# Kernel tuning notes

Measured on AMD Instinct MI355X. Metric: run time of the kernel, lower is better.

The kernel has to match this reference:

```python
import jax, jax.numpy as jnp
import numpy as np

B, K, U, I, D = 16384, 64, 100000, 100000, 256

def setup_inputs() -> dict:
    key = jax.random.key(0)
    k1, k2, k3, k4, k5, k6, k7, k8 = jax.random.split(key, 8)
    return {
        "nodes_u": jax.random.randint(k1, (B,), 0, U),
        "nodes_v": jax.random.randint(k2, (B,), 0, I),
        "neighbors": jax.random.randint(k3, (B, K), 0, U),
        "neighbor_counts": jax.random.randint(k4, (B,), 0, K + 1),
        "u2e": jax.random.normal(k5, (U, D), dtype=jnp.float32),
        "v2e": jax.random.normal(k6, (I, D), dtype=jnp.float32),
        "W": jax.random.normal(k7, (D, 2 * D), dtype=jnp.float32) * 0.05,  # torch Linear weight [out, in]
        "b": jax.random.normal(k8, (D,), dtype=jnp.float32) * 0.05,
    }

def reference(nodes_u, nodes_v, neighbors, neighbor_counts, u2e, v2e, W, b):
    # self embeddings [B, D]
    self_emb = u2e[nodes_u]
    # gather padded neighbor embeddings [B, K, D]
    neib_emb = u2e[neighbors]
    k_ = neighbors.shape[1]
    mask = jnp.arange(k_)[None, :] < neighbor_counts[:, None]          # [B, K] valid-neighbor mask
    nsum = jnp.einsum('bkd,bk->bd', neib_emb, mask.astype(neib_emb.dtype))
    cnt = jnp.maximum(neighbor_counts, 1).astype(self_emb.dtype)[:, None]
    nmean = nsum / cnt                                                  # mean-pool over valid neighbors
    cat = jnp.concatenate([self_emb, nmean], axis=1)                    # [B, 2D]
    proj = cat @ W.T + b                                                # Linear(2D -> D)
    # users with no neighbors use raw self embedding (matches `if len(neibs) > 0` branch)
    uemb = jnp.where((neighbor_counts > 0)[:, None], proj, self_emb)
    scores = jnp.sum(uemb * v2e[nodes_v], axis=1)                       # [B]
    return scores
```

## Files before the change

### kernel.cpp

```cpp
#include <hip/hip_runtime.h>

#define B_ROWS   16384
#define K_NB     64
#define D_DIM    256
#define TWO_D    512
#define R_BLK    8
#define THREADS  256

__global__ __launch_bounds__(THREADS, 4)
void easyrec_fused(const int* __restrict__ nodes_u,
                   const int* __restrict__ nodes_v,
                   const int* __restrict__ neighbors,
                   const int* __restrict__ neighbor_counts,
                   const float* __restrict__ u2e,
                   const float* __restrict__ v2e,
                   const float* __restrict__ W,
                   const float* __restrict__ bias,
                   float* __restrict__ out)
{
    __shared__ __align__(16) int   nbr_lds[R_BLK * K_NB];
    __shared__ __align__(16) float cat_lds[R_BLK][TWO_D];
    __shared__ float red_lds[R_BLK * 4];
    __shared__ float selfdot_lds[R_BLK];
    __shared__ float bdot_lds[R_BLK];

    const int t    = threadIdx.x;
    const int wave = t >> 6;
    const int lane = t & 63;
    const int row0 = blockIdx.x * R_BLK;

    nbr_lds[t]           = neighbors[(size_t)row0 * K_NB + t];
    nbr_lds[t + THREADS] = neighbors[(size_t)row0 * K_NB + t + THREADS];
    __syncthreads();

    const unsigned colb = (unsigned)lane * 16u;

    {
        const float4 b4 = *(const float4*)((const char*)bias + colb);
        #pragma unroll
        for (int rr = 0; rr < 2; ++rr) {
            const int r   = wave + rr * 4;
            const int row = row0 + r;
            const int nu  = __builtin_amdgcn_readfirstlane(nodes_u[row]);
            const int nv  = __builtin_amdgcn_readfirstlane(nodes_v[row]);
            const float4 self4 = *(const float4*)((const char*)u2e + (((unsigned)nu) << 10) + colb);
            const float4 v4    = *(const float4*)((const char*)v2e + (((unsigned)nv) << 10) + colb);
            *(float4*)(&cat_lds[r][4 * lane]) = self4;
            float sv = self4.x * v4.x + self4.y * v4.y + self4.z * v4.z + self4.w * v4.w;
            float bv = b4.x * v4.x + b4.y * v4.y + b4.z * v4.z + b4.w * v4.w;
            #pragma unroll
            for (int off = 32; off > 0; off >>= 1) {
                sv += __shfl_xor(sv, off, 64);
                bv += __shfl_xor(bv, off, 64);
            }
            if (lane == 0) { selfdot_lds[r] = sv; bdot_lds[r] = bv; }
        }
    }

    const int rowA = row0 + wave, rowB = rowA + 4;
    const int cntA = __builtin_amdgcn_readfirstlane(neighbor_counts[rowA]);
    const int cntB = __builtin_amdgcn_readfirstlane(neighbor_counts[rowB]);
    const int itA = (cntA + 7) >> 3;
    const int itB = (cntB + 7) >> 3;
    const int itMin = itA < itB ? itA : itB;
    const int itMax = itA > itB ? itA : itB;
    const int baseA = wave * K_NB;
    const int baseB = baseA + 4 * K_NB;

#define LOAD8(P, BASE, KK)                                                          \
    const int4 P##ia = *(const int4*)&nbr_lds[(BASE) + (KK)];                       \
    const int4 P##ib = *(const int4*)&nbr_lds[(BASE) + (KK) + 4];                   \
    const float4 P##n0 = *(const float4*)((const char*)u2e + (((unsigned)P##ia.x) << 10) + colb); \
    const float4 P##n1 = *(const float4*)((const char*)u2e + (((unsigned)P##ia.y) << 10) + colb); \
    const float4 P##n2 = *(const float4*)((const char*)u2e + (((unsigned)P##ia.z) << 10) + colb); \
    const float4 P##n3 = *(const float4*)((const char*)u2e + (((unsigned)P##ia.w) << 10) + colb); \
    const float4 P##n4 = *(const float4*)((const char*)u2e + (((unsigned)P##ib.x) << 10) + colb); \
    const float4 P##n5 = *(const float4*)((const char*)u2e + (((unsigned)P##ib.y) << 10) + colb); \
    const float4 P##n6 = *(const float4*)((const char*)u2e + (((unsigned)P##ib.z) << 10) + colb); \
    const float4 P##n7 = *(const float4*)((const char*)u2e + (((unsigned)P##ib.w) << 10) + colb);

#define ACC8(P, ACC, CNT, KK)                                                       \
    {                                                                               \
        const float m0 = ((KK) + 0 < (CNT)) ? 1.f : 0.f;                            \
        const float m1 = ((KK) + 1 < (CNT)) ? 1.f : 0.f;                            \
        const float m2 = ((KK) + 2 < (CNT)) ? 1.f : 0.f;                            \
        const float m3 = ((KK) + 3 < (CNT)) ? 1.f : 0.f;                            \
        const float m4 = ((KK) + 4 < (CNT)) ? 1.f : 0.f;                            \
        const float m5 = ((KK) + 5 < (CNT)) ? 1.f : 0.f;                            \
        const float m6 = ((KK) + 6 < (CNT)) ? 1.f : 0.f;                            \
        const float m7 = ((KK) + 7 < (CNT)) ? 1.f : 0.f;                            \
        ACC.x += m0*P##n0.x + m1*P##n1.x + m2*P##n2.x + m3*P##n3.x                  \
               + m4*P##n4.x + m5*P##n5.x + m6*P##n6.x + m7*P##n7.x;                 \
        ACC.y += m0*P##n0.y + m1*P##n1.y + m2*P##n2.y + m3*P##n3.y                  \
               + m4*P##n4.y + m5*P##n5.y + m6*P##n6.y + m7*P##n7.y;                 \
        ACC.z += m0*P##n0.z + m1*P##n1.z + m2*P##n2.z + m3*P##n3.z                  \
               + m4*P##n4.z + m5*P##n5.z + m6*P##n6.z + m7*P##n7.z;                 \
        ACC.w += m0*P##n0.w + m1*P##n1.w + m2*P##n2.w + m3*P##n3.w                  \
               + m4*P##n4.w + m5*P##n5.w + m6*P##n6.w + m7*P##n7.w;                 \
    }

    float4 accA = make_float4(0.f, 0.f, 0.f, 0.f);
    float4 accB = make_float4(0.f, 0.f, 0.f, 0.f);

    for (int i = 0; i < itMin; ++i) {
        const int k = i << 3;
        LOAD8(A, baseA, k)
        LOAD8(B, baseB, k)
        ACC8(A, accA, cntA, k)
        ACC8(B, accB, cntB, k)
    }
    if (itMin < itMax) {
        const bool Along = itA > itB;
        const int  cntL  = Along ? cntA : cntB;
        const int  baseL = Along ? baseA : baseB;
        float4 accL = make_float4(0.f, 0.f, 0.f, 0.f);
        for (int i = itMin; i < itMax; ++i) {
            const int k = i << 3;
            LOAD8(L, baseL, k)
            ACC8(L, accL, cntL, k)
        }
        if (Along) {
            accA.x += accL.x; accA.y += accL.y; accA.z += accL.z; accA.w += accL.w;
        } else {
            accB.x += accL.x; accB.y += accL.y; accB.z += accL.z; accB.w += accL.w;
        }
    }
#undef LOAD8
#undef ACC8

    {
        const float invA = 1.0f / (float)(cntA > 0 ? cntA : 1);
        const float invB = 1.0f / (float)(cntB > 0 ? cntB : 1);
        *(float4*)(&cat_lds[wave][D_DIM + 4 * lane]) =
            make_float4(accA.x * invA, accA.y * invA, accA.z * invA, accA.w * invA);
        *(float4*)(&cat_lds[wave + 4][D_DIM + 4 * lane]) =
            make_float4(accB.x * invB, accB.y * invB, accB.z * invB, accB.w * invB);
    }
    __syncthreads();

    unsigned voff[R_BLK];
    #pragma unroll
    for (int r = 0; r < R_BLK; ++r) {
        const int nv = __builtin_amdgcn_readfirstlane(nodes_v[row0 + r]);
        voff[r] = ((unsigned)nv) << 10;
    }

    float2 acc2[R_BLK];
    #pragma unroll
    for (int r = 0; r < R_BLK; ++r) acc2[r] = make_float2(0.f, 0.f);

    const unsigned tb8 = (unsigned)t * 8u;
    for (int d = 0; d < D_DIM; d += 4) {
        float4 vq[R_BLK];
        #pragma unroll
        for (int r = 0; r < R_BLK; ++r)
            vq[r] = *(const float4*)((const char*)v2e + voff[r] + (unsigned)d * 4u);

        #pragma unroll
        for (int dd = 0; dd < 4; ++dd) {
            const float2 wq = *(const float2*)((const char*)W + (((unsigned)(d + dd)) << 11) + tb8);
            #pragma unroll
            for (int r = 0; r < R_BLK; ++r) {
                const float vs = (dd == 0) ? vq[r].x : (dd == 1) ? vq[r].y
                               : (dd == 2) ? vq[r].z : vq[r].w;
                acc2[r].x += wq.x * vs;
                acc2[r].y += wq.y * vs;
            }
        }
    }

    #pragma unroll
    for (int r = 0; r < R_BLK; ++r) {
        const float2 c2 = *(const float2*)(&cat_lds[r][2 * t]);
        float p = c2.x * acc2[r].x + c2.y * acc2[r].y;
        #pragma unroll
        for (int off = 32; off > 0; off >>= 1) p += __shfl_xor(p, off, 64);
        if (lane == 0) red_lds[r * 4 + wave] = p;
    }
    __syncthreads();

    if (t < R_BLK) {
        const int row = row0 + t;
        const int cnt = neighbor_counts[row];
        float s;
        if (cnt > 0) {
            s = red_lds[t * 4 + 0] + red_lds[t * 4 + 1]
              + red_lds[t * 4 + 2] + red_lds[t * 4 + 3] + bdot_lds[t];
        } else {
            s = selfdot_lds[t];
        }
        out[row] = s;
    }
}

extern "C" void kernel_launch(void* const* d_in, const int* in_sizes, int n_in,
                              void* d_out, int out_size, void* d_ws, size_t ws_size,
                              hipStream_t stream) {
    const int*   nodes_u         = (const int*)d_in[0];
    const int*   nodes_v         = (const int*)d_in[1];
    const int*   neighbors       = (const int*)d_in[2];
    const int*   neighbor_counts = (const int*)d_in[3];
    const float* u2e             = (const float*)d_in[4];
    const float* v2e             = (const float*)d_in[5];
    const float* W               = (const float*)d_in[6];
    const float* bias            = (const float*)d_in[7];
    float*       out             = (float*)d_out;

    const int blocks = B_ROWS / R_BLK;
    easyrec_fused<<<blocks, THREADS, 0, stream>>>(
        nodes_u, nodes_v, neighbors, neighbor_counts, u2e, v2e, W, bias, out);
}
```

Measured before the change: 327.3 us.

## Gather neighbor embeddings from a per-call fp16 copy of the user table

Adds a pre-pass kernel that converts the whole u2e table to fp16 in the workspace. The fused kernel then gathers neighbor rows at half the byte count, widening them back to fp32 before accumulating. This targets the memory traffic of the mean-pool gather, the dominant cost. In exchange, every call pays to stream the full table (read fp32, write fp16), and neighbor means lose precision. A restructured fp32 fallback kernel runs when the workspace is too small.

```diff
diff --git a/kernel.cpp b/kernel.cpp
--- a/kernel.cpp
+++ b/kernel.cpp
@@ -1,22 +1,41 @@
 #include <hip/hip_runtime.h>
+#include <hip/hip_fp16.h>
 
 #define B_ROWS   16384
 #define K_NB     64
+#define U_ROWS   100000
 #define D_DIM    256
 #define TWO_D    512
 #define R_BLK    8
 #define THREADS  256
 
+__global__ __launch_bounds__(256)
+void cvt_u2e_fp16(const float* __restrict__ src, __half* __restrict__ dst, int n8) {
+    const int i = blockIdx.x * 256 + threadIdx.x;
+    if (i >= n8) return;
+    const float4 a = ((const float4*)src)[2 * i];
+    const float4 b = ((const float4*)src)[2 * i + 1];
+    const __half2 h0 = __floats2half2_rn(a.x, a.y);
+    const __half2 h1 = __floats2half2_rn(a.z, a.w);
+    const __half2 h2 = __floats2half2_rn(b.x, b.y);
+    const __half2 h3 = __floats2half2_rn(b.z, b.w);
+    int4 o;
+    o.x = *(const int*)&h0; o.y = *(const int*)&h1;
+    o.z = *(const int*)&h2; o.w = *(const int*)&h3;
+    ((int4*)dst)[i] = o;
+}
+
 __global__ __launch_bounds__(THREADS, 4)
-void easyrec_fused(const int* __restrict__ nodes_u,
-                   const int* __restrict__ nodes_v,
-                   const int* __restrict__ neighbors,
-                   const int* __restrict__ neighbor_counts,
-                   const float* __restrict__ u2e,
-                   const float* __restrict__ v2e,
-                   const float* __restrict__ W,
-                   const float* __restrict__ bias,
-                   float* __restrict__ out)
+void easyrec_fused_h(const int* __restrict__ nodes_u,
+                     const int* __restrict__ nodes_v,
+                     const int* __restrict__ neighbors,
+                     const int* __restrict__ neighbor_counts,
+                     const float* __restrict__ u2e,
+                     const __half* __restrict__ uh,
+                     const float* __restrict__ v2e,
+                     const float* __restrict__ W,
+                     const float* __restrict__ bias,
+                     float* __restrict__ out)
 {
     __shared__ __align__(16) int   nbr_lds[R_BLK * K_NB];
     __shared__ __align__(16) float cat_lds[R_BLK][TWO_D];
@@ -34,6 +53,7 @@
     __syncthreads();
 
     const unsigned colb = (unsigned)lane * 16u;
+    const unsigned colh = (unsigned)lane * 8u;
 
     {
         const float4 b4 = *(const float4*)((const char*)bias + colb);
@@ -43,8 +63,8 @@
             const int row = row0 + r;
             const int nu  = __builtin_amdgcn_readfirstlane(nodes_u[row]);
             const int nv  = __builtin_amdgcn_readfirstlane(nodes_v[row]);
-            const float4 self4 = *(const float4*)((const char*)u2e + (((unsigned)nu) << 10) + colb);
-            const float4 v4    = *(const float4*)((const char*)v2e + (((unsigned)nv) << 10) + colb);
+            const float4 self4 = *(const float4*)((const char*)u2e + (((size_t)nu) << 10) + colb);
+            const float4 v4    = *(const float4*)((const char*)v2e + (((size_t)nv) << 10) + colb);
             *(float4*)(&cat_lds[r][4 * lane]) = self4;
             float sv = self4.x * v4.x + self4.y * v4.y + self4.z * v4.z + self4.w * v4.w;
             float bv = b4.x * v4.x + b4.y * v4.y + b4.z * v4.z + b4.w * v4.w;
@@ -67,19 +87,29 @@
     const int baseA = wave * K_NB;
     const int baseB = baseA + 4 * K_NB;
 
-#define LOAD8(P, BASE, KK)                                                          \
+#define LOADH8(P, BASE, KK)                                                         \
     const int4 P##ia = *(const int4*)&nbr_lds[(BASE) + (KK)];                       \
     const int4 P##ib = *(const int4*)&nbr_lds[(BASE) + (KK) + 4];                   \
-    const float4 P##n0 = *(const float4*)((const char*)u2e + (((unsigned)P##ia.x) << 10) + colb); \
-    const float4 P##n1 = *(const float4*)((const char*)u2e + (((unsigned)P##ia.y) << 10) + colb); \
-    const float4 P##n2 = *(const float4*)((const char*)u2e + (((unsigned)P##ia.z) << 10) + colb); \
-    const float4 P##n3 = *(const float4*)((const char*)u2e + (((unsigned)P##ia.w) << 10) + colb); \
-    const float4 P##n4 = *(const float4*)((const char*)u2e + (((unsigned)P##ib.x) << 10) + colb); \
-    const float4 P##n5 = *(const float4*)((const char*)u2e + (((unsigned)P##ib.y) << 10) + colb); \
-    const float4 P##n6 = *(const float4*)((const char*)u2e + (((unsigned)P##ib.z) << 10) + colb); \
-    const float4 P##n7 = *(const float4*)((const char*)u2e + (((unsigned)P##ib.w) << 10) + colb);
-
-#define ACC8(P, ACC, CNT, KK)                                                       \
+    const uint2 P##n0 = *(const uint2*)((const char*)uh + (((unsigned)P##ia.x) << 9) + colh); \
+    const uint2 P##n1 = *(const uint2*)((const char*)uh + (((unsigned)P##ia.y) << 9) + colh); \
+    const uint2 P##n2 = *(const uint2*)((const char*)uh + (((unsigned)P##ia.z) << 9) + colh); \
+    const uint2 P##n3 = *(const uint2*)((const char*)uh + (((unsigned)P##ia.w) << 9) + colh); \
+    const uint2 P##n4 = *(const uint2*)((const char*)uh + (((unsigned)P##ib.x) << 9) + colh); \
+    const uint2 P##n5 = *(const uint2*)((const char*)uh + (((unsigned)P##ib.y) << 9) + colh); \
+    const uint2 P##n6 = *(const uint2*)((const char*)uh + (((unsigned)P##ib.z) << 9) + colh); \
+    const uint2 P##n7 = *(const uint2*)((const char*)uh + (((unsigned)P##ib.w) << 9) + colh);
+
+#define H2F_LO(u) __half22float2(*(const __half2*)&(u))
+
+#define ACCH1(P, N, ACC, M)                                                         \
+    {                                                                               \
+        const float2 f_a = H2F_LO(P##N.x);                                          \
+        const float2 f_b = H2F_LO(P##N.y);                                          \
+        ACC.x += (M) * f_a.x; ACC.y += (M) * f_a.y;                                 \
+        ACC.z += (M) * f_b.x; ACC.w += (M) * f_b.y;                                 \
+    }
+
+#define ACCH8(P, ACC, CNT, KK)                                                      \
     {                                                                               \
         const float m0 = ((KK) + 0 < (CNT)) ? 1.f : 0.f;                            \
         const float m1 = ((KK) + 1 < (CNT)) ? 1.f : 0.f;                            \
@@ -89,14 +119,10 @@
         const float m5 = ((KK) + 5 < (CNT)) ? 1.f : 0.f;                            \
         const float m6 = ((KK) + 6 < (CNT)) ? 1.f : 0.f;                            \
         const float m7 = ((KK) + 7 < (CNT)) ? 1.f : 0.f;                            \
-        ACC.x += m0*P##n0.x + m1*P##n1.x + m2*P##n2.x + m3*P##n3.x                  \
-               + m4*P##n4.x + m5*P##n5.x + m6*P##n6.x + m7*P##n7.x;                 \
-        ACC.y += m0*P##n0.y + m1*P##n1.y + m2*P##n2.y + m3*P##n3.y                  \
-               + m4*P##n4.y + m5*P##n5.y + m6*P##n6.y + m7*P##n7.y;                 \
-        ACC.z += m0*P##n0.z + m1*P##n1.z + m2*P##n2.z + m3*P##n3.z                  \
-               + m4*P##n4.z + m5*P##n5.z + m6*P##n6.z + m7*P##n7.z;                 \
-        ACC.w += m0*P##n0.w + m1*P##n1.w + m2*P##n2.w + m3*P##n3.w                  \
-               + m4*P##n4.w + m5*P##n5.w + m6*P##n6.w + m7*P##n7.w;                 \
+        ACCH1(P, n0, ACC, m0) ACCH1(P, n1, ACC, m1)                                 \
+        ACCH1(P, n2, ACC, m2) ACCH1(P, n3, ACC, m3)                                 \
+        ACCH1(P, n4, ACC, m4) ACCH1(P, n5, ACC, m5)                                 \
+        ACCH1(P, n6, ACC, m6) ACCH1(P, n7, ACC, m7)                                 \
     }
 
     float4 accA = make_float4(0.f, 0.f, 0.f, 0.f);
@@ -104,10 +130,10 @@
 
     for (int i = 0; i < itMin; ++i) {
         const int k = i << 3;
-        LOAD8(A, baseA, k)
-        LOAD8(B, baseB, k)
-        ACC8(A, accA, cntA, k)
-        ACC8(B, accB, cntB, k)
+        LOADH8(A, baseA, k)
+        LOADH8(B, baseB, k)
+        ACCH8(A, accA, cntA, k)
+        ACCH8(B, accB, cntB, k)
     }
     if (itMin < itMax) {
         const bool Along = itA > itB;
@@ -116,8 +142,8 @@
         float4 accL = make_float4(0.f, 0.f, 0.f, 0.f);
         for (int i = itMin; i < itMax; ++i) {
             const int k = i << 3;
-            LOAD8(L, baseL, k)
-            ACC8(L, accL, cntL, k)
+            LOADH8(L, baseL, k)
+            ACCH8(L, accL, cntL, k)
         }
         if (Along) {
             accA.x += accL.x; accA.y += accL.y; accA.z += accL.z; accA.w += accL.w;
@@ -125,8 +151,10 @@
             accB.x += accL.x; accB.y += accL.y; accB.z += accL.z; accB.w += accL.w;
         }
     }
-#undef LOAD8
-#undef ACC8
+#undef LOADH8
+#undef ACCH8
+#undef ACCH1
+#undef H2F_LO
 
     {
         const float invA = 1.0f / (float)(cntA > 0 ? cntA : 1);
@@ -159,6 +187,138 @@
         #pragma unroll
         for (int dd = 0; dd < 4; ++dd) {
             const float2 wq = *(const float2*)((const char*)W + (((unsigned)(d + dd)) << 11) + tb8);
+            #pragma unroll
+            for (int r = 0; r < R_BLK; ++r) {
+                const float vs = (dd == 0) ? vq[r].x : (dd == 1) ? vq[r].y
+                               : (dd == 2) ? vq[r].z : vq[r].w;
+                acc2[r].x += wq.x * vs;
+                acc2[r].y += wq.y * vs;
+            }
+        }
+    }
+
+    #pragma unroll
+    for (int r = 0; r < R_BLK; ++r) {
+        const float2 c2 = *(const float2*)(&cat_lds[r][2 * t]);
+        float p = c2.x * acc2[r].x + c2.y * acc2[r].y;
+        #pragma unroll
+        for (int off = 32; off > 0; off >>= 1) p += __shfl_xor(p, off, 64);
+        if (lane == 0) red_lds[r * 4 + wave] = p;
+    }
+    __syncthreads();
+
+    if (t < R_BLK) {
+        const int row = row0 + t;
+        const int cnt = neighbor_counts[row];
+        float s;
+        if (cnt > 0) {
+            s = red_lds[t * 4 + 0] + red_lds[t * 4 + 1]
+              + red_lds[t * 4 + 2] + red_lds[t * 4 + 3] + bdot_lds[t];
+        } else {
+            s = selfdot_lds[t];
+        }
+        out[row] = s;
+    }
+}
+
+__global__ __launch_bounds__(THREADS, 4)
+void easyrec_fused_f(const int* __restrict__ nodes_u,
+                     const int* __restrict__ nodes_v,
+                     const int* __restrict__ neighbors,
+                     const int* __restrict__ neighbor_counts,
+                     const float* __restrict__ u2e,
+                     const float* __restrict__ v2e,
+                     const float* __restrict__ W,
+                     const float* __restrict__ bias,
+                     float* __restrict__ out)
+{
+    __shared__ __align__(16) int   nbr_lds[R_BLK * K_NB];
+    __shared__ __align__(16) float cat_lds[R_BLK][TWO_D];
+    __shared__ float red_lds[R_BLK * 4];
+    __shared__ float selfdot_lds[R_BLK];
+    __shared__ float bdot_lds[R_BLK];
+
+    const int t    = threadIdx.x;
+    const int wave = t >> 6;
+    const int lane = t & 63;
+    const int row0 = blockIdx.x * R_BLK;
+
+    nbr_lds[t]           = neighbors[(size_t)row0 * K_NB + t];
+    nbr_lds[t + THREADS] = neighbors[(size_t)row0 * K_NB + t + THREADS];
+    __syncthreads();
+
+    for (int rr = 0; rr < 2; ++rr) {
+        const int r   = wave + rr * 4;
+        const int row = row0 + r;
+        const int nu  = __builtin_amdgcn_readfirstlane(nodes_u[row]);
+        const int nv  = __builtin_amdgcn_readfirstlane(nodes_v[row]);
+        const int cnt = __builtin_amdgcn_readfirstlane(neighbor_counts[row]);
+
+        const float4 self4 = *(const float4*)(u2e + (size_t)nu * D_DIM + 4 * lane);
+        const float4 v4    = *(const float4*)(v2e + (size_t)nv * D_DIM + 4 * lane);
+        const float4 b4    = *(const float4*)(bias + 4 * lane);
+
+        float4 acc = make_float4(0.f, 0.f, 0.f, 0.f);
+        const int base = r * K_NB;
+        const int kmax = (cnt + 7) & ~7;
+        for (int k = 0; k < kmax; k += 8) {
+            const int4 ia = *(const int4*)&nbr_lds[base + k];
+            const int4 ib = *(const int4*)&nbr_lds[base + k + 4];
+            const float4 n0 = *(const float4*)(u2e + (size_t)ia.x * D_DIM + 4 * lane);
+            const float4 n1 = *(const float4*)(u2e + (size_t)ia.y * D_DIM + 4 * lane);
+            const float4 n2 = *(const float4*)(u2e + (size_t)ia.z * D_DIM + 4 * lane);
+            const float4 n3 = *(const float4*)(u2e + (size_t)ia.w * D_DIM + 4 * lane);
+            const float4 n4 = *(const float4*)(u2e + (size_t)ib.x * D_DIM + 4 * lane);
+            const float4 n5 = *(const float4*)(u2e + (size_t)ib.y * D_DIM + 4 * lane);
+            const float4 n6 = *(const float4*)(u2e + (size_t)ib.z * D_DIM + 4 * lane);
+            const float4 n7 = *(const float4*)(u2e + (size_t)ib.w * D_DIM + 4 * lane);
+            const float m0 = (k + 0 < cnt) ? 1.f : 0.f;
+            const float m1 = (k + 1 < cnt) ? 1.f : 0.f;
+            const float m2 = (k + 2 < cnt) ? 1.f : 0.f;
+            const float m3 = (k + 3 < cnt) ? 1.f : 0.f;
+            const float m4 = (k + 4 < cnt) ? 1.f : 0.f;
+            const float m5 = (k + 5 < cnt) ? 1.f : 0.f;
+            const float m6 = (k + 6 < cnt) ? 1.f : 0.f;
+            const float m7 = (k + 7 < cnt) ? 1.f : 0.f;
+            acc.x += n0.x*m0 + n1.x*m1 + n2.x*m2 + n3.x*m3 + n4.x*m4 + n5.x*m5 + n6.x*m6 + n7.x*m7;
+            acc.y += n0.y*m0 + n1.y*m1 + n2.y*m2 + n3.y*m3 + n4.y*m4 + n5.y*m5 + n6.y*m6 + n7.y*m7;
+            acc.z += n0.z*m0 + n1.z*m1 + n2.z*m2 + n3.z*m3 + n4.z*m4 + n5.z*m5 + n6.z*m6 + n7.z*m7;
+            acc.w += n0.w*m0 + n1.w*m1 + n2.w*m2 + n3.w*m3 + n4.w*m4 + n5.w*m5 + n6.w*m6 + n7.w*m7;
+        }
+        const float inv = 1.0f / (float)(cnt > 0 ? cnt : 1);
+        *(float4*)(&cat_lds[r][4 * lane])         = self4;
+        *(float4*)(&cat_lds[r][D_DIM + 4 * lane]) =
+            make_float4(acc.x * inv, acc.y * inv, acc.z * inv, acc.w * inv);
+
+        float sv = self4.x * v4.x + self4.y * v4.y + self4.z * v4.z + self4.w * v4.w;
+        float bv = b4.x * v4.x + b4.y * v4.y + b4.z * v4.z + b4.w * v4.w;
+        #pragma unroll
+        for (int off = 32; off > 0; off >>= 1) {
+            sv += __shfl_xor(sv, off, 64);
+            bv += __shfl_xor(bv, off, 64);
+        }
+        if (lane == 0) { selfdot_lds[r] = sv; bdot_lds[r] = bv; }
+    }
+    __syncthreads();
+
+    const float* vrow[R_BLK];
+    #pragma unroll
+    for (int r = 0; r < R_BLK; ++r) {
+        const int nv = __builtin_amdgcn_readfirstlane(nodes_v[row0 + r]);
+        vrow[r] = v2e + (size_t)nv * D_DIM;
+    }
+
+    float2 acc2[R_BLK];
+    #pragma unroll
+    for (int r = 0; r < R_BLK; ++r) acc2[r] = make_float2(0.f, 0.f);
+
+    for (int d = 0; d < D_DIM; d += 4) {
+        float4 vq[R_BLK];
+        #pragma unroll
+        for (int r = 0; r < R_BLK; ++r) vq[r] = *(const float4*)(vrow[r] + d);
+        #pragma unroll
+        for (int dd = 0; dd < 4; ++dd) {
+            const float2 wq = *(const float2*)(W + (size_t)(d + dd) * TWO_D + 2 * t);
             #pragma unroll
             for (int r = 0; r < R_BLK; ++r) {
                 const float vs = (dd == 0) ? vq[r].x : (dd == 1) ? vq[r].y
@@ -206,7 +366,18 @@
     const float* bias            = (const float*)d_in[7];
     float*       out             = (float*)d_out;
 
+    const size_t need = (size_t)U_ROWS * D_DIM * sizeof(__half);
     const int blocks = B_ROWS / R_BLK;
-    easyrec_fused<<<blocks, THREADS, 0, stream>>>(
-        nodes_u, nodes_v, neighbors, neighbor_counts, u2e, v2e, W, bias, out);
+
+    if (d_ws != nullptr && ws_size >= need) {
+        __half* uh = (__half*)d_ws;
+        const int n8 = U_ROWS * D_DIM / 8;
+        const int cblocks = (n8 + 255) / 256;
+        cvt_u2e_fp16<<<cblocks, 256, 0, stream>>>(u2e, uh, n8);
+        easyrec_fused_h<<<blocks, THREADS, 0, stream>>>(
+            nodes_u, nodes_v, neighbors, neighbor_counts, u2e, uh, v2e, W, bias, out);
+    } else {
+        easyrec_fused_f<<<blocks, THREADS, 0, stream>>>(
+            nodes_u, nodes_v, neighbors, neighbor_counts, u2e, v2e, W, bias, out);
+    }
 }
```

After: 327.8 us. About the same (+0.1%).
